# Kernel tuning notes

Hardware: AMD Instinct MI355X
Metric: run time of the kernel (lower is better)

## Reference

```python
import jax, jax.numpy as jnp
import numpy as np

LOG2 = float(np.log(2.0))
HALF_LOG_2PI = 0.5 * float(np.log(2.0 * np.pi))


def softplus_b(x):
    # nn.Softplus(beta=log(2)): (1/beta)*log(1+exp(beta*x))
    return jax.nn.softplus(LOG2 * x) / LOG2


def setup_inputs() -> dict:
    key = jax.random.key(0)
    B, T, K, H, V = 32, 128, 256, 512, 10000
    ks = jax.random.split(key, 10)
    x = jax.random.randint(ks[0], (B, T), 0, V)
    x_sl = jax.random.randint(ks[1], (B,), 64, T + 1)  # lengths in [64, T]
    eps = jax.random.normal(ks[2], (B, T, K), dtype=jnp.float32)
    emb_weight = jax.random.normal(ks[3], (V, 2 * K), dtype=jnp.float32) * 0.02
    w_ih = jax.random.normal(ks[4], (4 * H, K), dtype=jnp.float32) * 0.02
    w_hh = jax.random.normal(ks[5], (4 * H, H), dtype=jnp.float32) * 0.02
    b_ih = jnp.zeros((4 * H,), jnp.float32)
    b_hh = jnp.zeros((4 * H,), jnp.float32)
    w_prior = jax.random.normal(ks[6], (V, H), dtype=jnp.float32) * 0.02
    b_prior = jnp.zeros((V,), jnp.float32)
    w_gen = jax.random.normal(ks[7], (V, K), dtype=jnp.float32) * 0.02
    b_gen = jnp.zeros((V,), jnp.float32)
    return dict(x=x, x_sl=x_sl, eps=eps, emb_weight=emb_weight, w_ih=w_ih, w_hh=w_hh,
                b_ih=b_ih, b_hh=b_hh, w_prior=w_prior, b_prior=b_prior,
                w_gen=w_gen, b_gen=b_gen)


def _lstm(z, w_ih, w_hh, b_ih, b_hh):
    # z: (B,T,K) -> h: (B,T,H); PyTorch gate order i,f,g,o
    B, T, _ = z.shape
    H = w_hh.shape[1]
    x_proj = jnp.einsum('btk,gk->btg', z, w_ih) + b_ih + b_hh  # (B,T,4H)

    def step(carry, xt):
        h, c = carry
        gates = xt + h @ w_hh.T
        i, f, g, o = jnp.split(gates, 4, axis=-1)
        c = jax.nn.sigmoid(f) * c + jax.nn.sigmoid(i) * jnp.tanh(g)
        h = jax.nn.sigmoid(o) * jnp.tanh(c)
        return (h, c), h

    init = (jnp.zeros((B, H), z.dtype), jnp.zeros((B, H), z.dtype))
    _, hs = jax.lax.scan(step, init, jnp.swapaxes(x_proj, 0, 1))
    return jnp.swapaxes(hs, 0, 1)


def reference(x, x_sl, eps, emb_weight, w_ih, w_hh, b_ih, b_hh,
              w_prior, b_prior, w_gen, b_gen):
    B, T = x.shape
    K = eps.shape[-1]
    dt = eps.dtype
    mask2 = (jnp.arange(T)[None, :] < x_sl[:, None]).astype(dt)  # (B,T)

    # infer: q(z|x) from embedding lookup
    e = emb_weight[x]                         # (B,T,2K)
    mu_q, sig_q = e[..., :K], softplus_b(e[..., K:])
    z = (mu_q + sig_q * eps) * mask2[:, :, None]  # rsample * mask

    # prior: LSTM over shifted z -> mixture weights over V components
    z_shift = jnp.concatenate([jnp.zeros((B, 1, K), dt), z[:, :-1]], axis=1)
    h = _lstm(z_shift, w_ih, w_hh, b_ih, b_hh)            # (B,T,H)
    logw = jax.nn.log_softmax(h @ w_prior.T + b_prior, axis=2)  # (B,T,V)

    # GMM component log-probs summed over K, expanded into GEMMs
    mu_p, sig_p = emb_weight[:, :K], softplus_b(emb_weight[:, K:])  # (V,K)
    inv2var = 0.5 / (sig_p * sig_p)
    const = jnp.sum(-HALF_LOG_2PI - jnp.log(sig_p) - mu_p * mu_p * inv2var, axis=1)  # (V,)
    lp = (const[None, None, :]
          + jnp.einsum('btk,vk->btv', z, 2.0 * inv2var * mu_p)
          - jnp.einsum('btk,vk->btv', z * z, inv2var))     # (B,T,V)
    p_z_lp = jax.nn.logsumexp(logw + lp, axis=2)           # (B,T)

    q_z_lp = jnp.sum(-HALF_LOG_2PI - jnp.log(sig_q)
                     - 0.5 * ((z - mu_q) / sig_q) ** 2, axis=2)

    kl_bt = (q_z_lp - p_z_lp) * mask2

    # reconstruction: categorical log-likelihood of x
    logits_x = z @ w_gen.T + b_gen                         # (B,T,V)
    log_px = jnp.take_along_axis(jax.nn.log_softmax(logits_x, axis=2),
                                 x[..., None], axis=2)[..., 0] * mask2

    kl = kl_bt.sum(axis=1)
    log_prob = log_px.sum(axis=1)
    loss = -((log_prob - kl).sum() / x_sl.sum().astype(dt))  # beta=1.0
    return loss
```

## Files before the change

kernel.cpp:

```cpp
#include <hip/hip_runtime.h>
#include <hip/hip_bf16.h>
#include <math.h>

#define BB 32
#define TT 128
#define KK 256
#define HH 512
#define VV 10000
#define VP 10240
#define BT 4096
#define HLOG2PI 0.91893853320467274178f
#define FMSHIFT 16.0f


typedef short bf16x8 __attribute__((ext_vector_type(8)));
typedef float f32x4 __attribute__((ext_vector_type(4)));

__device__ __forceinline__ float softplus_b(float x) {
    float ax = fabsf(x);
    return fmaxf(x, 0.0f) + log2f(1.0f + exp2f(-ax));
}
__device__ __forceinline__ float sigm(float x) { return 1.0f / (1.0f + expf(-x)); }
__device__ __forceinline__ float fsigm(float x) { return 1.0f / (1.0f + __expf(-x)); }
__device__ __forceinline__ float ftanh(float x) {
    float e = __expf(2.0f * x);
    return 1.0f - 2.0f / (e + 1.0f);
}
__device__ __forceinline__ unsigned short f2bf(float f) {
    unsigned u = __float_as_uint(f);
    u += 0x7FFFu + ((u >> 16) & 1u);
    return (unsigned short)(u >> 16);
}
typedef _Float16 h2f16 __attribute__((ext_vector_type(2)));
__device__ __forceinline__ unsigned pkh2(float a, float b) {
    h2f16 h;
    h.x = (_Float16)a;
    h.y = (_Float16)b;
    return *(unsigned*)&h;
}
__device__ __forceinline__ float fdot2u(unsigned a, unsigned b, float c) {
    h2f16 ah = *(h2f16*)&a, bh = *(h2f16*)&b;
#if __has_builtin(__builtin_amdgcn_fdot2)
    return __builtin_amdgcn_fdot2(ah, bh, c, false);
#else
    return c + (float)ah.x * (float)bh.x + (float)ah.y * (float)bh.y;
#endif
}
__device__ __forceinline__ bf16x8 bsq(bf16x8 a) {
    union { bf16x8 v; unsigned w[4]; } u, r;
    u.v = a;
#pragma unroll
    for (int i = 0; i < 4; i++) {
        float lo = __uint_as_float(u.w[i] << 16);
        float hi = __uint_as_float(u.w[i] & 0xFFFF0000u);
        lo *= lo;
        hi *= hi;
        asm("v_cvt_pk_bf16_f32 %0, %1, %2" : "=v"(r.w[i]) : "v"(lo), "v"(hi));
    }
    return r.v;
}

__global__ void k_embed(const int* __restrict__ x, const int* __restrict__ x_sl,
                        const float* __restrict__ eps, const float* __restrict__ emb,
                        const float* __restrict__ w_gen, const float* __restrict__ b_gen,
                        ushort* __restrict__ zb, float* __restrict__ qz,
                        float* __restrict__ gx) {
    int bt = blockIdx.x;
    int b = bt >> 7, t = bt & 127;
    int k = threadIdx.x;
    int xi = x[bt];
    float e1 = emb[xi * 512 + k];
    float sg = softplus_b(emb[xi * 512 + 256 + k]);
    float ep = eps[bt * 256 + k];
    float mk = (t < x_sl[b]) ? 1.f : 0.f;
    float zv = (e1 + sg * ep) * mk;
    zb[bt * 256 + k] = f2bf(zv);
    float q = -HLOG2PI - logf(sg) - 0.5f * ep * ep;
    float p = zv * w_gen[xi * 256 + k];
    __shared__ float red[256];
    red[k] = q;
    __syncthreads();
    for (int s = 128; s > 0; s >>= 1) {
        if (k < s) red[k] += red[k + s];
        __syncthreads();
    }
    if (k == 0) qz[bt] = red[0];
    __syncthreads();
    red[k] = p;
    __syncthreads();
    for (int s = 128; s > 0; s >>= 1) {
        if (k < s) red[k] += red[k + s];
        __syncthreads();
    }
    if (k == 0) gx[bt] = red[0] + b_gen[xi];
}

__global__ __launch_bounds__(512) void k_xpm(const ushort* __restrict__ zb,
                                             const ushort* __restrict__ wb,
                                             const float* __restrict__ b_ih,
                                             const float* __restrict__ b_hh,
                                             float* __restrict__ xp) {
    __shared__ ushort zs[16384];
    int tid = threadIdx.x;
    int mb = blockIdx.x >> 3;
    int nb = blockIdx.x & 7;
    int bt0 = mb << 6;
    int n0base = nb << 8;
    for (int i = tid; i < 2048; i += 512) {
        int quad = i & 3, row = (i >> 2) & 63, kc = i >> 8;
        int bt = bt0 + row;
        uint4 v = make_uint4(0, 0, 0, 0);
        if ((bt & 127) != 0)
            v = *(const uint4*)(zb + (size_t)(bt - 1) * 256 + kc * 32 + quad * 8);
        int g = (((row << 2) + (quad ^ (row & 3))) ^ (((row >> 2) & 1) << 2));
        *(uint4*)(zs + kc * 2048 + g * 8) = v;
    }
    __syncthreads();
    int w = tid >> 6, l = tid & 63;
    int quad = l >> 4, ln = l & 15;
    int n0 = n0base + (w << 5);
    const bf16x8* zs8 = (const bf16x8*)zs;
    const bf16x8* wb8 = (const bf16x8*)wb;
    int g0 = (((ln << 2) + (quad ^ (ln & 3))) ^ (((ln >> 2) & 1) << 2));
    int rb = (n0 + ln) << 5;
    f32x4 acc[4][2];
#pragma unroll
    for (int ns = 0; ns < 2; ns++) {
        int col = n0 + (ns << 4) + ln;
        float bias = b_ih[col] + b_hh[col];
#pragma unroll
        for (int ms = 0; ms < 4; ms++) acc[ms][ns] = bias;
    }
#pragma unroll
    for (int kc = 0; kc < 8; kc++) {
        bf16x8 b0 = wb8[rb + (kc << 2) + quad];
        bf16x8 b1 = wb8[rb + 512 + (kc << 2) + quad];
#pragma unroll
        for (int ms = 0; ms < 4; ms++) {
            bf16x8 a = zs8[(kc << 8) + g0 + (ms << 6)];
            acc[ms][0] = __builtin_amdgcn_mfma_f32_16x16x32_bf16(a, b0, acc[ms][0], 0, 0, 0);
            acc[ms][1] = __builtin_amdgcn_mfma_f32_16x16x32_bf16(a, b1, acc[ms][1], 0, 0, 0);
        }
    }
#pragma unroll
    for (int ms = 0; ms < 4; ms++)
#pragma unroll
        for (int ns = 0; ns < 2; ns++)
#pragma unroll
            for (int r = 0; r < 4; r++) {
                int row = bt0 + (ms << 4) + (quad << 2) + r;
                xp[(size_t)row * 2048 + n0 + (ns << 4) + ln] = acc[ms][ns][r];
            }
}

__global__ __launch_bounds__(256) void k_wpack2(const float* __restrict__ w_hh,
                                                uint4* __restrict__ wpIF,
                                                uint4* __restrict__ wpGO) {
    int o = blockIdx.x * 256 + threadIdx.x;
    if (blockIdx.y == 0) {
        int kq = o & 3, j_local = (o >> 2) & 63, q = (o >> 8) & 31, m = o >> 13;
        int jg = (m << 6) + j_local;
        int k = (kq << 7) + (q << 2);
        const float* wi = w_hh + (size_t)jg * 512 + k;
        const float* wf = w_hh + (size_t)(512 + jg) * 512 + k;
        uint4 u;
        u.x = pkh2(wi[0], wi[1]); u.y = pkh2(wi[2], wi[3]);
        u.z = pkh2(wf[0], wf[1]); u.w = pkh2(wf[2], wf[3]);
        wpIF[o] = u;
    } else {
        int q = o & 31, kq = (o >> 5) & 3, j_local = (o >> 7) & 63, m = o >> 13;
        int jg = (m << 6) + j_local;
        int k = (kq << 7) + (q << 2);
        const float* wg = w_hh + (size_t)(1024 + jg) * 512 + k;
        const float* wo = w_hh + (size_t)(1536 + jg) * 512 + k;
        uint4 u;
        u.x = pkh2(wg[0], wg[1]); u.y = pkh2(wg[2], wg[3]);
        u.z = pkh2(wo[0], wo[1]); u.w = pkh2(wo[2], wo[3]);
        wpGO[o] = u;
    }
}

__global__ __launch_bounds__(256, 1) void k_lstm(const float* __restrict__ xp,
                                                 const uint4* __restrict__ wpIF,
                                                 const uint4* __restrict__ wpGO,
                                                 ushort* __restrict__ h_all,
                                                 unsigned* __restrict__ hpk) {
    extern __shared__ char smc[];
    uint4* wif = (uint4*)smc;
    unsigned* hs2 = (unsigned*)(smc + 131072);
    int bid = blockIdx.x;
    int b = bid & 31;
    int m = bid >> 5;
    int tid = threadIdx.x;
    int w = tid >> 6, l = tid & 63;
    int jj = l >> 2, kq = l & 3;
    int j_local = (w << 4) + jj;
    int j_global = (m << 6) + j_local;
    const uint4* srcIF = wpIF + ((size_t)m << 13);
    for (int i = tid; i < 8192; i += 256) wif[i] = srcIF[i];
    uint4 wgo[32];
    const uint4* srcGO = wpGO + ((size_t)((((m << 6) + j_local) << 2) + kq) << 5);
#pragma unroll
    for (int q = 0; q < 32; q++) wgo[q] = srcGO[q];
    const uint4* wifp = wif + (w << 6) + l;
    int skslot = tid + ((tid >> 6) << 2);
    float c = 0.f;
    __syncthreads();
    for (int t = 0; t < 128; t++) {
        int bt = (b << 7) + t;
        float xg0 = 0.f, xg1 = 0.f, xg2 = 0.f, xg3 = 0.f;
        if (kq == 0) {
            const float* xpr = xp + (size_t)bt * 2048 + j_global;
            xg0 = xpr[0]; xg1 = xpr[512]; xg2 = xpr[1024]; xg3 = xpr[1536];
        }
        float a0 = 0.f, a1 = 0.f, a2 = 0.f, a3 = 0.f;
        if (t > 0) {
            const unsigned* src = hpk + ((size_t)(bt - 1) << 8);
            unsigned u;
            do {
                u = __hip_atomic_load(src + tid, __ATOMIC_RELAXED, __HIP_MEMORY_SCOPE_AGENT);
            } while (u == 0xFFFFFFFFu);
            unsigned* hbuf = hs2 + ((t - 1) & 1) * 272;
            hbuf[skslot] = u;
            __syncthreads();
            const unsigned* hp2 = hbuf + kq * 68;
#pragma unroll
            for (int q = 0; q < 32; q++) {
                uint4 A = wifp[q << 8];
                uint4 B = wgo[q];
                unsigned p0 = hp2[q << 1];
                unsigned p1 = hp2[(q << 1) + 1];
                a0 = fdot2u(A.x, p0, a0); a0 = fdot2u(A.y, p1, a0);
                a1 = fdot2u(A.z, p0, a1); a1 = fdot2u(A.w, p1, a1);
                a2 = fdot2u(B.x, p0, a2); a2 = fdot2u(B.y, p1, a2);
                a3 = fdot2u(B.z, p0, a3); a3 = fdot2u(B.w, p1, a3);
            }
#pragma unroll
            for (int off = 1; off <= 2; off <<= 1) {
                a0 += __shfl_xor(a0, off);
                a1 += __shfl_xor(a1, off);
                a2 += __shfl_xor(a2, off);
                a3 += __shfl_xor(a3, off);
            }
        }
        float h = 0.f;
        if (kq == 0) {
            float g0 = xg0 + a0, g1 = xg1 + a1, g2 = xg2 + a2, g3 = xg3 + a3;
            c = fsigm(g1) * c + fsigm(g0) * ftanh(g2);
            h = fsigm(g3) * ftanh(c);
            h_all[(size_t)bt * 512 + j_global] = f2bf(h);
        }
        float hp = __shfl_xor(h, 4);
        if (kq == 0 && (jj & 1) == 0) {
            unsigned u = pkh2(h, hp);
            __hip_atomic_store(hpk + ((size_t)bt << 8) + (m << 5) + (w << 3) + (jj >> 1),
                               u, __ATOMIC_RELAXED, __HIP_MEMORY_SCOPE_AGENT);
        }
    }
}

__global__ __launch_bounds__(256) void k_pack_w(const float* __restrict__ src,
                                                ushort* __restrict__ dst, int kshift) {
    int o = blockIdx.x * 256 + threadIdx.x;
    int c = o & ((1 << kshift) - 1);
    int r = o >> kshift;
    ushort4 u = make_ushort4(0, 0, 0, 0);
    if (r < VV) {
        float4 v = *(const float4*)(src + ((size_t)r << (kshift + 2)) + (c << 2));
        u = make_ushort4(f2bf(v.x), f2bf(v.y), f2bf(v.z), f2bf(v.w));
    }
    *(ushort4*)(dst + ((size_t)o << 2)) = u;
}

__global__ void k_pack_q(const float* __restrict__ emb, ushort* __restrict__ Qb,
                         float* __restrict__ cv) {
    int v = blockIdx.x, k = threadIdx.x;
    if (v >= VV) {
        Qb[((size_t)v << 9) + k] = 0;
        Qb[((size_t)v << 9) + 256 + k] = 0;
        if (k == 0) cv[v] = 0.f;
        return;
    }
    float mu = emb[(size_t)v * 512 + k];
    float sg = softplus_b(emb[(size_t)v * 512 + 256 + k]);
    float iv = 0.5f / (sg * sg);
    Qb[((size_t)v << 9) + k] = f2bf(2.f * iv * mu);
    Qb[((size_t)v << 9) + 256 + k] = f2bf(-iv);
    float ct = -HLOG2PI - logf(sg) - mu * mu * iv;
    __shared__ float red[256];
    red[k] = ct;
    __syncthreads();
    for (int s = 128; s > 0; s >>= 1) {
        if (k < s) red[k] += red[k + s];
        __syncthreads();
    }
    if (k == 0) cv[v] = red[0];
}

__global__ __launch_bounds__(512, 2) void k_scores(
    const ushort* __restrict__ hb, const ushort* __restrict__ zb,
    const ushort* __restrict__ Pb, const ushort* __restrict__ Qb,
    const ushort* __restrict__ Gb, const float* __restrict__ cv,
    const float* __restrict__ b_prior, const float* __restrict__ b_gen,
    float* __restrict__ part) {
    extern __shared__ ushort sm[];
    ushort* hT = sm;
    ushort* fzT = sm + 32768;
    int tid = threadIdx.x;
    int vs = blockIdx.x & 7;
    int mb = blockIdx.x >> 3;
    int bt0 = mb << 6;
    int vbase = vs * 1280;
    for (int i = tid; i < 4096; i += 512) {
        int quad = i & 3, row = (i >> 2) & 63, kc = i >> 8;
        uint4 v = *(const uint4*)(hb + (size_t)(bt0 + row) * 512 + kc * 32 + quad * 8);
        int g = (((row << 2) + (quad ^ (row & 3))) ^ (((row >> 2) & 1) << 2));
        *(uint4*)(hT + kc * 2048 + g * 8) = v;
    }
    for (int i = tid; i < 2048; i += 512) {
        int quad = i & 3, row = (i >> 2) & 63, kc = i >> 8;
        uint4 v = *(const uint4*)(zb + (size_t)(bt0 + row) * 256 + kc * 32 + quad * 8);
        int g = (((row << 2) + (quad ^ (row & 3))) ^ (((row >> 2) & 1) << 2));
        *(uint4*)(fzT + kc * 2048 + g * 8) = v;
        bf16x8 sq = bsq(*(bf16x8*)&v);
        *(uint4*)(fzT + (kc + 8) * 2048 + g * 8) = *(uint4*)&sq;
    }
    __syncthreads();
    int w = tid >> 6, l = tid & 63;
    int quad = l >> 4, ln = l & 15;
    int nq = w;
    const bf16x8* hT8 = (const bf16x8*)hT;
    const bf16x8* fz8 = (const bf16x8*)fzT;
    const bf16x8* Pb8 = (const bf16x8*)Pb;
    const bf16x8* Qb8 = (const bf16x8*)Qb;
    const bf16x8* Gb8 = (const bf16x8*)Gb;
    int g0 = (((ln << 2) + (quad ^ (ln & 3))) ^ (((ln >> 2) & 1) << 2));
    float Ls[3][16], Lm1[16];
#pragma unroll
    for (int c = 0; c < 3; c++)
#pragma unroll
        for (int r = 0; r < 16; r++) Ls[c][r] = 0.f;
#pragma unroll
    for (int r = 0; r < 16; r++) Lm1[r] = -1e30f;
#pragma unroll 1
    for (int nt = 0; nt < 5; nt++) {
        int n0 = vbase + (nt << 8) + (nq << 5);
        int rb = (n0 + ln) << 6;
        int rg = (n0 + ln) << 5;
        __builtin_amdgcn_s_setprio(1);
        f32x4 accA[4][2];
#pragma unroll
        for (int ms = 0; ms < 4; ms++) { accA[ms][0] = 0.f; accA[ms][1] = 0.f; }
#pragma unroll 2
        for (int kc = 0; kc < 16; kc++) {
            bf16x8 b0 = Pb8[rb + (kc << 2) + quad];
            bf16x8 b1 = Pb8[rb + 1024 + (kc << 2) + quad];
#pragma unroll
            for (int ms = 0; ms < 4; ms++) {
                bf16x8 a = hT8[(kc << 8) + g0 + (ms << 6)];
                accA[ms][0] = __builtin_amdgcn_mfma_f32_16x16x32_bf16(a, b0, accA[ms][0], 0, 0, 0);
                accA[ms][1] = __builtin_amdgcn_mfma_f32_16x16x32_bf16(a, b1, accA[ms][1], 0, 0, 0);
            }
        }
        __builtin_amdgcn_s_setprio(0);
        f32x4 accB[4][2];
#pragma unroll
        for (int ns = 0; ns < 2; ns++) {
            int col = n0 + (ns << 4) + ln;
            bool ok = col < VV;
            float bpv = ok ? b_prior[col] : 0.f;
            float cvv = ok ? cv[col] : 0.f;
#pragma unroll
            for (int ms = 0; ms < 4; ms++)
#pragma unroll
                for (int r = 0; r < 4; r++) {
                    int r16 = (ms << 2) + r;
                    float u1 = ok ? accA[ms][ns][r] + bpv : -1e30f;
                    Ls[0][r16] += __expf(u1 - FMSHIFT);
                    accB[ms][ns][r] = ok ? u1 + cvv : -1e30f;
                }
        }
        __builtin_amdgcn_s_setprio(1);
#pragma unroll 2
        for (int kc = 0; kc < 16; kc++) {
            bf16x8 bq0 = Qb8[rb + (kc << 2) + quad];
            bf16x8 bq1 = Qb8[rb + 1024 + (kc << 2) + quad];
#pragma unroll
            for (int ms = 0; ms < 4; ms++) {
                bf16x8 a = fz8[(kc << 8) + g0 + (ms << 6)];
                accB[ms][0] = __builtin_amdgcn_mfma_f32_16x16x32_bf16(a, bq0, accB[ms][0], 0, 0, 0);
                accB[ms][1] = __builtin_amdgcn_mfma_f32_16x16x32_bf16(a, bq1, accB[ms][1], 0, 0, 0);
            }
        }
        __builtin_amdgcn_s_setprio(0);
#pragma unroll
        for (int ns = 0; ns < 2; ns++)
#pragma unroll
            for (int ms = 0; ms < 4; ms++)
#pragma unroll
                for (int r = 0; r < 4; r++) {
                    int r16 = (ms << 2) + r;
                    float u2 = accB[ms][ns][r];
                    float nm = fmaxf(Lm1[r16], u2);
                    Ls[1][r16] = Ls[1][r16] * __expf(Lm1[r16] - nm) + __expf(u2 - nm);
                    Lm1[r16] = nm;
                }
        f32x4 accC[4][2];
#pragma unroll
        for (int ns = 0; ns < 2; ns++) {
            int col = n0 + (ns << 4) + ln;
            bool ok = col < VV;
            float bgv = ok ? b_gen[col] : -1e30f;
#pragma unroll
            for (int ms = 0; ms < 4; ms++) accC[ms][ns] = bgv;
        }
        __builtin_amdgcn_s_setprio(1);
#pragma unroll 2
        for (int kc = 0; kc < 8; kc++) {
            bf16x8 bg0 = Gb8[rg + (kc << 2) + quad];
            bf16x8 bg1 = Gb8[rg + 512 + (kc << 2) + quad];
#pragma unroll
            for (int ms = 0; ms < 4; ms++) {
                bf16x8 a = fz8[(kc << 8) + g0 + (ms << 6)];
                accC[ms][0] = __builtin_amdgcn_mfma_f32_16x16x32_bf16(a, bg0, accC[ms][0], 0, 0, 0);
                accC[ms][1] = __builtin_amdgcn_mfma_f32_16x16x32_bf16(a, bg1, accC[ms][1], 0, 0, 0);
            }
        }
        __builtin_amdgcn_s_setprio(0);
#pragma unroll
        for (int ns = 0; ns < 2; ns++)
#pragma unroll
            for (int ms = 0; ms < 4; ms++)
#pragma unroll
                for (int r = 0; r < 4; r++)
                    Ls[2][(ms << 2) + r] += __expf(accC[ms][ns][r] - FMSHIFT);
    }
#pragma unroll
    for (int off = 1; off <= 8; off <<= 1)
#pragma unroll
        for (int r16 = 0; r16 < 16; r16++) {
            Ls[0][r16] += __shfl_xor(Ls[0][r16], off);
            Ls[2][r16] += __shfl_xor(Ls[2][r16], off);
            float mo = __shfl_xor(Lm1[r16], off);
            float so = __shfl_xor(Ls[1][r16], off);
            float nm = fmaxf(Lm1[r16], mo);
            Ls[1][r16] = Ls[1][r16] * __expf(Lm1[r16] - nm) + so * __expf(mo - nm);
            Lm1[r16] = nm;
        }
    __syncthreads();
    float* bs = (float*)sm;
    float* bm = bs + 1536;
    if (ln == 0) {
#pragma unroll
        for (int r16 = 0; r16 < 16; r16++) {
            int row = ((r16 >> 2) << 4) + (quad << 2) + (r16 & 3);
#pragma unroll
            for (int c = 0; c < 3; c++) bs[(c * 8 + w) * 64 + row] = Ls[c][r16];
            bm[w * 64 + row] = Lm1[r16];
        }
    }
    __syncthreads();
    if (tid < 192) {
        int c = tid >> 6, row = tid & 63;
        float M, S;
        if (c == 1) {
            M = -1e30f; S = 0.f;
#pragma unroll
            for (int q = 0; q < 8; q++) {
                float m = bm[q * 64 + row];
                float s = bs[(8 + q) * 64 + row];
                float Mn = fmaxf(M, m);
                S = S * __expf(M - Mn) + s * __expf(m - Mn);
                M = Mn;
            }
        } else {
            M = FMSHIFT; S = 0.f;
#pragma unroll
            for (int q = 0; q < 8; q++) S += bs[(c * 8 + q) * 64 + row];
        }
        part[(vs * 6 + c * 2) * 4096 + bt0 + row] = M;
        part[(vs * 6 + c * 2 + 1) * 4096 + bt0 + row] = S;
    }
}

__device__ __forceinline__ float lse8(const float* __restrict__ part, int comp, int bt) {
    float M = -1e30f, S = 0.f;
#pragma unroll
    for (int vsi = 0; vsi < 8; vsi++) {
        float m = part[(vsi * 6 + comp) * 4096 + bt];
        float s = part[(vsi * 6 + comp + 1) * 4096 + bt];
        float Mn = fmaxf(M, m);
        S = S * __expf(M - Mn) + s * __expf(m - Mn);
        M = Mn;
    }
    return M + logf(S);
}

__global__ void k_final1(const float* __restrict__ part, const float* __restrict__ qz,
                         const float* __restrict__ gxv, const int* __restrict__ x_sl,
                         float* __restrict__ psum) {
    int bid = blockIdx.x;
    int tid = threadIdx.x;
    int bt = (bid << 7) + tid;
    float S = 0.f;
    if (tid < x_sl[bid]) {
        float lse1 = lse8(part, 0, bt);
        float lse2 = lse8(part, 2, bt);
        float lse3 = lse8(part, 4, bt);
        float p_z = lse2 - lse1;
        float kl = qz[bt] - p_z;
        float px = gxv[bt] - lse3;
        S = px - kl;
    }
    __shared__ float red[128];
    red[tid] = S;
    __syncthreads();
    for (int s = 64; s > 0; s >>= 1) {
        if (tid < s) red[tid] += red[tid + s];
        __syncthreads();
    }
    if (tid == 0) psum[bid] = red[0];
}

__global__ void k_final2(const float* __restrict__ psum, const int* __restrict__ x_sl,
                         float* __restrict__ out) {
    int tid = threadIdx.x;
    float s = (tid < 32) ? psum[tid] : 0.f;
#pragma unroll
    for (int off = 32; off >= 1; off >>= 1) s += __shfl_down(s, off);
    if (tid == 0) {
        int sl = 0;
        for (int b = 0; b < 32; b++) sl += x_sl[b];
        out[0] = -(s / (float)sl);
    }
}

extern "C" void kernel_launch(void* const* d_in, const int* in_sizes, int n_in,
                              void* d_out, int out_size, void* d_ws, size_t ws_size,
                              hipStream_t stream) {
    const int* x = (const int*)d_in[0];
    const int* x_sl = (const int*)d_in[1];
    const float* eps = (const float*)d_in[2];
    const float* emb = (const float*)d_in[3];
    const float* w_ih = (const float*)d_in[4];
    const float* w_hh = (const float*)d_in[5];
    const float* b_ih = (const float*)d_in[6];
    const float* b_hh = (const float*)d_in[7];
    const float* w_prior = (const float*)d_in[8];
    const float* b_prior = (const float*)d_in[9];
    const float* w_gen = (const float*)d_in[10];
    const float* b_gen = (const float*)d_in[11];

    float* ws = (float*)d_ws;
    float* qz = ws + 1048576;
    ushort* hb = (ushort*)(ws + 1052672);
    ushort* zb = (ushort*)(ws + 1052672 + 1048576);
    float* gx = ws + 3149824;
    float* region = ws + 3252224;
    float* xp = region;
    uint4* wpIF = (uint4*)(region + 8388608);
    uint4* wpGO = wpIF + 65536;
    unsigned* hpk = (unsigned*)(region + 8912896);
    ushort* wb = (ushort*)(region + 9961472);
    ushort* Pb = (ushort*)(region);
    ushort* Qb = (ushort*)(region + 2621440);
    ushort* Gb = (ushort*)(region + 5242880);
    float* part = region + 6553600;
    float* psum = region + 6750208;
    float* cv = region + 13107200;

    k_embed<<<4096, 256, 0, stream>>>(x, x_sl, eps, emb, w_gen, b_gen, zb, qz, gx);
    k_pack_w<<<512, 256, 0, stream>>>(w_ih, wb, 6);
    k_xpm<<<512, 512, 0, stream>>>(zb, wb, b_ih, b_hh, xp);
    k_wpack2<<<dim3(256, 2), 256, 0, stream>>>(w_hh, wpIF, wpGO);
    hipMemsetAsync(hpk, 0xFF, 4194304, stream);
    {
        hipFuncSetAttribute((const void*)k_lstm, hipFuncAttributeMaxDynamicSharedMemorySize, 133248);
        void* args[] = {(void*)&xp, (void*)&wpIF, (void*)&wpGO, (void*)&hb, (void*)&hpk};
        hipLaunchCooperativeKernel((const void*)k_lstm, dim3(256), dim3(256), args, 133248, stream);
    }
    k_pack_w<<<5120, 256, 0, stream>>>(w_prior, Pb, 7);
    k_pack_w<<<2560, 256, 0, stream>>>(w_gen, Gb, 6);
    k_pack_q<<<10240, 256, 0, stream>>>(emb, Qb, cv);
    hipFuncSetAttribute((const void*)k_scores, hipFuncAttributeMaxDynamicSharedMemorySize, 131072);
    k_scores<<<512, 512, 131072, stream>>>(hb, zb, Pb, Qb, Gb, cv, b_prior, b_gen, part);
    k_final1<<<32, 128, 0, stream>>>(part, qz, gx, x_sl, psum);
    k_final2<<<1, 64, 0, stream>>>(psum, x_sl, (float*)d_out);
}
```

Before: 717.7 us.

## Overlap weight packing with LSTM recurrence and store input projection as bf16

The LSTM kernel now runs 512 threads per block. The first 256 threads run the recurrence and the extra waves pack w_prior, w_gen and the GMM Q/const tables in the idle time between timesteps, which removes three separate packing launches from the serial chain. The input projection is also written as bf16 instead of fp32, halving its store and load traffic. The risks are that the extra waves compete for issue slots and bandwidth during the latency-critical recurrence, and the gate inputs lose precision.

```diff
diff --git a/kernel.cpp b/kernel.cpp
--- a/kernel.cpp
+++ b/kernel.cpp
@@ -20,7 +20,6 @@
     float ax = fabsf(x);
     return fmaxf(x, 0.0f) + log2f(1.0f + exp2f(-ax));
 }
-__device__ __forceinline__ float sigm(float x) { return 1.0f / (1.0f + expf(-x)); }
 __device__ __forceinline__ float fsigm(float x) { return 1.0f / (1.0f + __expf(-x)); }
 __device__ __forceinline__ float ftanh(float x) {
     float e = __expf(2.0f * x);
@@ -30,6 +29,9 @@
     unsigned u = __float_as_uint(f);
     u += 0x7FFFu + ((u >> 16) & 1u);
     return (unsigned short)(u >> 16);
+}
+__device__ __forceinline__ float bf2f(unsigned short u) {
+    return __uint_as_float(((unsigned)u) << 16);
 }
 typedef _Float16 h2f16 __attribute__((ext_vector_type(2)));
 __device__ __forceinline__ unsigned pkh2(float a, float b) {
@@ -99,7 +101,7 @@
                                              const ushort* __restrict__ wb,
                                              const float* __restrict__ b_ih,
                                              const float* __restrict__ b_hh,
-                                             float* __restrict__ xp) {
+                                             ushort* __restrict__ xpb) {
     __shared__ ushort zs[16384];
     int tid = threadIdx.x;
     int mb = blockIdx.x >> 3;
@@ -149,7 +151,7 @@
 #pragma unroll
             for (int r = 0; r < 4; r++) {
                 int row = bt0 + (ms << 4) + (quad << 2) + r;
-                xp[(size_t)row * 2048 + n0 + (ns << 4) + ln] = acc[ms][ns][r];
+                xpb[(size_t)row * 2048 + n0 + (ns << 4) + ln] = f2bf(acc[ms][ns][r]);
             }
 }
 
@@ -180,81 +182,141 @@
     }
 }
 
-__global__ __launch_bounds__(256, 1) void k_lstm(const float* __restrict__ xp,
-                                                 const uint4* __restrict__ wpIF,
-                                                 const uint4* __restrict__ wpGO,
-                                                 ushort* __restrict__ h_all,
-                                                 unsigned* __restrict__ hpk) {
+__global__ __launch_bounds__(512, 1) void k_lstm(
+    const ushort* __restrict__ xpb, const uint4* __restrict__ wpIF,
+    const uint4* __restrict__ wpGO, ushort* __restrict__ h_all,
+    unsigned* __restrict__ hpk,
+    const float* __restrict__ w_prior, const float* __restrict__ w_gen2,
+    const float* __restrict__ emb,
+    ushort* __restrict__ Pb, ushort* __restrict__ Qb, ushort* __restrict__ Gb,
+    float* __restrict__ cv) {
     extern __shared__ char smc[];
     uint4* wif = (uint4*)smc;
     unsigned* hs2 = (unsigned*)(smc + 131072);
     int bid = blockIdx.x;
-    int b = bid & 31;
-    int m = bid >> 5;
     int tid = threadIdx.x;
-    int w = tid >> 6, l = tid & 63;
-    int jj = l >> 2, kq = l & 3;
-    int j_local = (w << 4) + jj;
-    int j_global = (m << 6) + j_local;
-    const uint4* srcIF = wpIF + ((size_t)m << 13);
-    for (int i = tid; i < 8192; i += 256) wif[i] = srcIF[i];
-    uint4 wgo[32];
-    const uint4* srcGO = wpGO + ((size_t)((((m << 6) + j_local) << 2) + kq) << 5);
-#pragma unroll
-    for (int q = 0; q < 32; q++) wgo[q] = srcGO[q];
-    const uint4* wifp = wif + (w << 6) + l;
-    int skslot = tid + ((tid >> 6) << 2);
-    float c = 0.f;
-    __syncthreads();
-    for (int t = 0; t < 128; t++) {
-        int bt = (b << 7) + t;
-        float xg0 = 0.f, xg1 = 0.f, xg2 = 0.f, xg3 = 0.f;
-        if (kq == 0) {
-            const float* xpr = xp + (size_t)bt * 2048 + j_global;
-            xg0 = xpr[0]; xg1 = xpr[512]; xg2 = xpr[1024]; xg3 = xpr[1536];
-        }
-        float a0 = 0.f, a1 = 0.f, a2 = 0.f, a3 = 0.f;
-        if (t > 0) {
-            const unsigned* src = hpk + ((size_t)(bt - 1) << 8);
-            unsigned u;
-            do {
-                u = __hip_atomic_load(src + tid, __ATOMIC_RELAXED, __HIP_MEMORY_SCOPE_AGENT);
-            } while (u == 0xFFFFFFFFu);
-            unsigned* hbuf = hs2 + ((t - 1) & 1) * 272;
-            hbuf[skslot] = u;
+    const uint4* srcIF = wpIF + ((size_t)(bid >> 5) << 13);
+    for (int i = tid; i < 8192; i += 512) wif[i] = srcIF[i];
+    if (tid < 256) {
+        int b = bid & 31;
+        int m = bid >> 5;
+        int w = tid >> 6, l = tid & 63;
+        int jj = l >> 2, kq = l & 3;
+        int j_local = (w << 4) + jj;
+        int j_global = (m << 6) + j_local;
+        uint4 wgo[32];
+        const uint4* srcGO = wpGO + ((size_t)((((m << 6) + j_local) << 2) + kq) << 5);
+#pragma unroll
+        for (int q = 0; q < 32; q++) wgo[q] = srcGO[q];
+        const uint4* wifp = wif + (w << 6) + l;
+        int skslot = tid + ((tid >> 6) << 2);
+        float c = 0.f;
+        __syncthreads();
+        for (int t = 0; t < 128; t++) {
+            int bt = (b << 7) + t;
+            float xg0 = 0.f, xg1 = 0.f, xg2 = 0.f, xg3 = 0.f;
+            if (kq == 0) {
+                const ushort* xpr = xpb + (size_t)bt * 2048 + j_global;
+                xg0 = bf2f(xpr[0]); xg1 = bf2f(xpr[512]);
+                xg2 = bf2f(xpr[1024]); xg3 = bf2f(xpr[1536]);
+            }
+            float a0 = 0.f, a1 = 0.f, a2 = 0.f, a3 = 0.f;
+            if (t > 0) {
+                const unsigned* src = hpk + ((size_t)(bt - 1) << 8);
+                unsigned u;
+                do {
+                    u = __hip_atomic_load(src + tid, __ATOMIC_RELAXED, __HIP_MEMORY_SCOPE_AGENT);
+                } while (u == 0xFFFFFFFFu);
+                unsigned* hbuf = hs2 + ((t - 1) & 1) * 272;
+                hbuf[skslot] = u;
+                __syncthreads();
+                const unsigned* hp2 = hbuf + kq * 68;
+#pragma unroll
+                for (int q = 0; q < 32; q++) {
+                    uint4 A = wifp[q << 8];
+                    uint4 B = wgo[q];
+                    unsigned p0 = hp2[q << 1];
+                    unsigned p1 = hp2[(q << 1) + 1];
+                    a0 = fdot2u(A.x, p0, a0); a0 = fdot2u(A.y, p1, a0);
+                    a1 = fdot2u(A.z, p0, a1); a1 = fdot2u(A.w, p1, a1);
+                    a2 = fdot2u(B.x, p0, a2); a2 = fdot2u(B.y, p1, a2);
+                    a3 = fdot2u(B.z, p0, a3); a3 = fdot2u(B.w, p1, a3);
+                }
+#pragma unroll
+                for (int off = 1; off <= 2; off <<= 1) {
+                    a0 += __shfl_xor(a0, off);
+                    a1 += __shfl_xor(a1, off);
+                    a2 += __shfl_xor(a2, off);
+                    a3 += __shfl_xor(a3, off);
+                }
+            }
+            float h = 0.f;
+            if (kq == 0) {
+                float g0 = xg0 + a0, g1 = xg1 + a1, g2 = xg2 + a2, g3 = xg3 + a3;
+                c = fsigm(g1) * c + fsigm(g0) * ftanh(g2);
+                h = fsigm(g3) * ftanh(c);
+                h_all[(size_t)bt * 512 + j_global] = f2bf(h);
+            }
+            float hp = __shfl_xor(h, 4);
+            if (kq == 0 && (jj & 1) == 0) {
+                unsigned u = pkh2(h, hp);
+                __hip_atomic_store(hpk + ((size_t)bt << 8) + ((bid >> 5) << 5) + ((tid >> 6) << 3) + (jj >> 1),
+                                   u, __ATOMIC_RELAXED, __HIP_MEMORY_SCOPE_AGENT);
+            }
+        }
+    } else {
+        int ptid = tid - 256;
+        int pw = ptid >> 6, pl = ptid & 63;
+        int v0 = bid * 40;
+        __syncthreads();
+        for (int t = 1; t < 128; t++) {
+            if (t <= 20) {
+                int u = ptid;
+                int row = v0 + 2 * (t - 1) + (u >> 7);
+                int c4 = u & 127;
+                ushort4 o = make_ushort4(0, 0, 0, 0);
+                if (row < VV) {
+                    float4 v = *(const float4*)(w_prior + (size_t)row * 512 + c4 * 4);
+                    o = make_ushort4(f2bf(v.x), f2bf(v.y), f2bf(v.z), f2bf(v.w));
+                }
+                *(ushort4*)(Pb + (size_t)row * 512 + c4 * 4) = o;
+            } else if (t <= 30) {
+                int u = ptid;
+                int row = v0 + 4 * (t - 21) + (u >> 6);
+                int c4 = u & 63;
+                ushort4 o = make_ushort4(0, 0, 0, 0);
+                if (row < VV) {
+                    float4 v = *(const float4*)(w_gen2 + (size_t)row * 256 + c4 * 4);
+                    o = make_ushort4(f2bf(v.x), f2bf(v.y), f2bf(v.z), f2bf(v.w));
+                }
+                *(ushort4*)(Gb + (size_t)row * 256 + c4 * 4) = o;
+            } else if (t <= 40) {
+                int v = v0 + 4 * (t - 31) + pw;
+                float ct = 0.f;
+                if (v < VV) {
+#pragma unroll
+                    for (int pass = 0; pass < 4; pass++) {
+                        int k = pass * 64 + pl;
+                        float mu = emb[(size_t)v * 512 + k];
+                        float sg = softplus_b(emb[(size_t)v * 512 + 256 + k]);
+                        float iv = 0.5f / (sg * sg);
+                        Qb[((size_t)v << 9) + k] = f2bf(2.f * iv * mu);
+                        Qb[((size_t)v << 9) + 256 + k] = f2bf(-iv);
+                        ct += -HLOG2PI - logf(sg) - mu * mu * iv;
+                    }
+                } else {
+#pragma unroll
+                    for (int pass = 0; pass < 4; pass++) {
+                        int k = pass * 64 + pl;
+                        Qb[((size_t)v << 9) + k] = 0;
+                        Qb[((size_t)v << 9) + 256 + k] = 0;
+                    }
+                }
+#pragma unroll
+                for (int off = 1; off <= 32; off <<= 1) ct += __shfl_xor(ct, off);
+                if (pl == 0) cv[v] = (v < VV) ? ct : 0.f;
+            }
             __syncthreads();
-            const unsigned* hp2 = hbuf + kq * 68;
-#pragma unroll
-            for (int q = 0; q < 32; q++) {
-                uint4 A = wifp[q << 8];
-                uint4 B = wgo[q];
-                unsigned p0 = hp2[q << 1];
-                unsigned p1 = hp2[(q << 1) + 1];
-                a0 = fdot2u(A.x, p0, a0); a0 = fdot2u(A.y, p1, a0);
-                a1 = fdot2u(A.z, p0, a1); a1 = fdot2u(A.w, p1, a1);
-                a2 = fdot2u(B.x, p0, a2); a2 = fdot2u(B.y, p1, a2);
-                a3 = fdot2u(B.z, p0, a3); a3 = fdot2u(B.w, p1, a3);
-            }
-#pragma unroll
-            for (int off = 1; off <= 2; off <<= 1) {
-                a0 += __shfl_xor(a0, off);
-                a1 += __shfl_xor(a1, off);
-                a2 += __shfl_xor(a2, off);
-                a3 += __shfl_xor(a3, off);
-            }
-        }
-        float h = 0.f;
-        if (kq == 0) {
-            float g0 = xg0 + a0, g1 = xg1 + a1, g2 = xg2 + a2, g3 = xg3 + a3;
-            c = fsigm(g1) * c + fsigm(g0) * ftanh(g2);
-            h = fsigm(g3) * ftanh(c);
-            h_all[(size_t)bt * 512 + j_global] = f2bf(h);
-        }
-        float hp = __shfl_xor(h, 4);
-        if (kq == 0 && (jj & 1) == 0) {
-            unsigned u = pkh2(h, hp);
-            __hip_atomic_store(hpk + ((size_t)bt << 8) + (m << 5) + (w << 3) + (jj >> 1),
-                               u, __ATOMIC_RELAXED, __HIP_MEMORY_SCOPE_AGENT);
         }
     }
 }
@@ -270,31 +332,6 @@
         u = make_ushort4(f2bf(v.x), f2bf(v.y), f2bf(v.z), f2bf(v.w));
     }
     *(ushort4*)(dst + ((size_t)o << 2)) = u;
-}
-
-__global__ void k_pack_q(const float* __restrict__ emb, ushort* __restrict__ Qb,
-                         float* __restrict__ cv) {
-    int v = blockIdx.x, k = threadIdx.x;
-    if (v >= VV) {
-        Qb[((size_t)v << 9) + k] = 0;
-        Qb[((size_t)v << 9) + 256 + k] = 0;
-        if (k == 0) cv[v] = 0.f;
-        return;
-    }
-    float mu = emb[(size_t)v * 512 + k];
-    float sg = softplus_b(emb[(size_t)v * 512 + 256 + k]);
-    float iv = 0.5f / (sg * sg);
-    Qb[((size_t)v << 9) + k] = f2bf(2.f * iv * mu);
-    Qb[((size_t)v << 9) + 256 + k] = f2bf(-iv);
-    float ct = -HLOG2PI - logf(sg) - mu * mu * iv;
-    __shared__ float red[256];
-    red[k] = ct;
-    __syncthreads();
-    for (int s = 128; s > 0; s >>= 1) {
-        if (k < s) red[k] += red[k + s];
-        __syncthreads();
-    }
-    if (k == 0) cv[v] = red[0];
 }
 
 __global__ __launch_bounds__(512, 2) void k_scores(
@@ -557,31 +594,30 @@
     ushort* zb = (ushort*)(ws + 1052672 + 1048576);
     float* gx = ws + 3149824;
     float* region = ws + 3252224;
-    float* xp = region;
-    uint4* wpIF = (uint4*)(region + 8388608);
+    ushort* xpb = (ushort*)region;
+    uint4* wpIF = (uint4*)(region + 4194304);
     uint4* wpGO = wpIF + 65536;
-    unsigned* hpk = (unsigned*)(region + 8912896);
-    ushort* wb = (ushort*)(region + 9961472);
-    ushort* Pb = (ushort*)(region);
-    ushort* Qb = (ushort*)(region + 2621440);
-    ushort* Gb = (ushort*)(region + 5242880);
-    float* part = region + 6553600;
-    float* psum = region + 6750208;
-    float* cv = region + 13107200;
+    unsigned* hpk = (unsigned*)(region + 4718592);
+    ushort* wb = (ushort*)(region + 5767168);
+    ushort* Pb = (ushort*)(region + 6029312);
+    ushort* Qb = (ushort*)(region + 8650752);
+    ushort* Gb = (ushort*)(region + 11272192);
+    float* part = region + 12582912;
+    float* psum = region + 12779520;
+    float* cv = region + 12779552;
 
     k_embed<<<4096, 256, 0, stream>>>(x, x_sl, eps, emb, w_gen, b_gen, zb, qz, gx);
     k_pack_w<<<512, 256, 0, stream>>>(w_ih, wb, 6);
-    k_xpm<<<512, 512, 0, stream>>>(zb, wb, b_ih, b_hh, xp);
+    k_xpm<<<512, 512, 0, stream>>>(zb, wb, b_ih, b_hh, xpb);
     k_wpack2<<<dim3(256, 2), 256, 0, stream>>>(w_hh, wpIF, wpGO);
     hipMemsetAsync(hpk, 0xFF, 4194304, stream);
     {
         hipFuncSetAttribute((const void*)k_lstm, hipFuncAttributeMaxDynamicSharedMemorySize, 133248);
-        void* args[] = {(void*)&xp, (void*)&wpIF, (void*)&wpGO, (void*)&hb, (void*)&hpk};
-        hipLaunchCooperativeKernel((const void*)k_lstm, dim3(256), dim3(256), args, 133248, stream);
-    }
-    k_pack_w<<<5120, 256, 0, stream>>>(w_prior, Pb, 7);
-    k_pack_w<<<2560, 256, 0, stream>>>(w_gen, Gb, 6);
-    k_pack_q<<<10240, 256, 0, stream>>>(emb, Qb, cv);
+        void* args[] = {(void*)&xpb, (void*)&wpIF, (void*)&wpGO, (void*)&hb, (void*)&hpk,
+                        (void*)&w_prior, (void*)&w_gen, (void*)&emb,
+                        (void*)&Pb, (void*)&Qb, (void*)&Gb, (void*)&cv};
+        hipLaunchCooperativeKernel((const void*)k_lstm, dim3(256), dim3(512), args, 133248, stream);
+    }
     hipFuncSetAttribute((const void*)k_scores, hipFuncAttributeMaxDynamicSharedMemorySize, 131072);
     k_scores<<<512, 512, 131072, stream>>>(hb, zb, Pb, Qb, Gb, cv, b_prior, b_gen, part);
     k_final1<<<32, 128, 0, stream>>>(part, qz, gx, x_sl, psum);
```

New measurement: 676.4 us. 5.8% less time.
